# Kernel tuning notes

Hardware: AMD Instinct MI355X
Metric: run time of the kernel (lower is better)

The kernel has to match this reference:

```python
import jax, jax.numpy as jnp
import numpy as np

D_MODEL = 1024
NUM_HEADS = 16
DFF = 4096
LN_EPS = 1e-08
CLIP = 10.0


def setup_inputs() -> dict:
    key = jax.random.key(0)
    ks = jax.random.split(key, 12)
    d, h, f = D_MODEL, NUM_HEADS, DFF
    s = 1.0 / np.sqrt(d)
    inp = {
        "x": jax.random.normal(ks[0], (4, 2048, d), dtype=jnp.float32),
        "wq": jax.random.normal(ks[1], (d, d), dtype=jnp.float32) * s,
        "bq": jnp.zeros((d,), jnp.float32),
        "wk": jax.random.normal(ks[2], (d, d), dtype=jnp.float32) * s,
        "bk": jnp.zeros((d,), jnp.float32),
        "wv": jax.random.normal(ks[3], (d, d), dtype=jnp.float32) * s,
        "bv": jnp.zeros((d,), jnp.float32),
        "wo": jax.random.normal(ks[4], (d, d), dtype=jnp.float32) * s,
        "bo": jnp.zeros((d,), jnp.float32),
        "w1": jax.random.normal(ks[5], (d, f), dtype=jnp.float32) * s,
        "b1": jnp.zeros((f,), jnp.float32),
        "w2": jax.random.normal(ks[6], (f, d), dtype=jnp.float32) * (1.0 / np.sqrt(f)),
        "b2": jnp.zeros((d,), jnp.float32),
        "ln_gamma": jnp.ones((d,), jnp.float32),
        "ln_beta": jnp.zeros((d,), jnp.float32),
    }
    return inp


def layernorm(x, gamma, beta):
    mu = jnp.mean(x, axis=-1, keepdims=True)
    var = jnp.var(x, axis=-1, keepdims=True)
    return (x - mu) * jax.lax.rsqrt(var + LN_EPS) * gamma + beta


def encoder_layer(x, wq, bq, wk, bk, wv, bv, wo, bo, w1, b1, w2, b2, ln_gamma, ln_beta):
    B, S, d = x.shape
    H = NUM_HEADS
    Dh = d // H
    q = (x @ wq + bq).reshape(B, S, H, Dh).transpose(0, 2, 1, 3)  # bhsd
    k = (x @ wk + bk).reshape(B, S, H, Dh).transpose(0, 2, 1, 3)
    v = (x @ wv + bv).reshape(B, S, H, Dh).transpose(0, 2, 1, 3)
    logits = jnp.einsum('bhqd,bhkd->bhqk', q, k) / jnp.sqrt(jnp.float32(Dh))
    logits = jnp.clip(logits, -CLIP, CLIP)
    attn = jax.nn.softmax(logits, axis=-1)
    ctx = jnp.einsum('bhqk,bhkd->bhqd', attn, v)
    ctx = ctx.transpose(0, 2, 1, 3).reshape(B, S, d)
    attn_out = ctx @ wo + bo
    out1 = layernorm(x + attn_out, ln_gamma, ln_beta)
    ffn = jax.nn.relu(out1 @ w1 + b1) @ w2 + b2
    return layernorm(out1 + ffn, ln_gamma, ln_beta)


def reference(x, wq, bq, wk, bk, wv, bv, wo, bo, w1, b1, w2, b2, ln_gamma, ln_beta):
    return encoder_layer(x, wq, bq, wk, bk, wv, bv, wo, bo, w1, b1, w2, b2, ln_gamma, ln_beta)
```

## Files before the change

### kernel.cpp

```cpp
#include <hip/hip_runtime.h>
#include <stdint.h>

#define D_MODEL 1024
#define NHEAD 16
#define DH 64
#define DFF 4096
#define BATCH 4
#define SEQ 2048
#define MTOT (BATCH*SEQ)

#define QSCALE 0.18033688011112043f
#define CLIP2  14.426950408889634f

typedef short short8 __attribute__((ext_vector_type(8)));
typedef float f32x4 __attribute__((ext_vector_type(4)));
typedef unsigned int uint;

__device__ inline unsigned short f2bf(float f) {
  union { float f; unsigned u; } v; v.f = f;
  unsigned r = v.u + 0x7fffu + ((v.u >> 16) & 1u);
  return (unsigned short)(r >> 16);
}
__device__ inline float bf2f(unsigned short b) {
  union { unsigned u; float f; } v; v.u = ((unsigned)b) << 16;
  return v.f;
}
__device__ inline unsigned pack_trunc(float lo, float hi) {
  union { float f; unsigned u; } a, b; a.f = lo; b.f = hi;
  return __builtin_amdgcn_perm(b.u, a.u, 0x07060302u);
}
__device__ __forceinline__ void async16(const unsigned short* g, unsigned short* l) {
  __builtin_amdgcn_global_load_lds(
      (const __attribute__((address_space(1))) unsigned int*)g,
      (__attribute__((address_space(3))) unsigned int*)l, 16, 0, 0);
}

__global__ void cast_kernel(const float* __restrict__ in, unsigned short* __restrict__ out, int n4) {
  int i = blockIdx.x * blockDim.x + threadIdx.x;
  if (i < n4) {
    float4 v = ((const float4*)in)[i];
    ushort4 o;
    o.x = f2bf(v.x); o.y = f2bf(v.y); o.z = f2bf(v.z); o.w = f2bf(v.w);
    ((ushort4*)out)[i] = o;
  }
}

__global__ void transpose_weights_kernel(
    const float* __restrict__ wq, const float* __restrict__ wk,
    const float* __restrict__ wv, const float* __restrict__ wo,
    const float* __restrict__ w1, const float* __restrict__ w2,
    unsigned short* __restrict__ wqkvT, unsigned short* __restrict__ woT,
    unsigned short* __restrict__ w1T, unsigned short* __restrict__ w2T) {
  __shared__ unsigned short tile[32][33];
  const int id = blockIdx.x;
  const float* in; unsigned short* out; int K, N, n0, k0; float scale = 1.0f;
  if (id < 4096) {
    const int wi = id >> 10, t = id & 1023;
    switch (wi) {
      case 0:  in = wq; out = wqkvT;           scale = QSCALE; break;
      case 1:  in = wk; out = wqkvT + 1048576; break;
      case 2:  in = wv; out = wqkvT + 2097152; break;
      default: in = wo; out = woT;             break;
    }
    K = 1024; N = 1024; n0 = (t & 31) * 32; k0 = (t >> 5) * 32;
  } else if (id < 8192) {
    const int t = id - 4096;
    in = w1; out = w1T; K = 1024; N = 4096; n0 = (t & 127) * 32; k0 = (t >> 7) * 32;
  } else {
    const int t = id - 8192;
    in = w2; out = w2T; K = 4096; N = 1024; n0 = (t & 31) * 32; k0 = (t >> 5) * 32;
  }
  const int tx = threadIdx.x & 31, ty = threadIdx.x >> 5;
#pragma unroll
  for (int j = 0; j < 32; j += 8)
    tile[ty + j][tx] = f2bf(in[(size_t)(k0 + ty + j) * N + n0 + tx] * scale);
  __syncthreads();
#pragma unroll
  for (int j = 0; j < 32; j += 8)
    out[(size_t)(n0 + ty + j) * K + k0 + tx] = tile[tx][ty + j];
}

__global__ void bias_concat_kernel(const float* __restrict__ bq, const float* __restrict__ bk,
                                   const float* __restrict__ bv, float* __restrict__ o) {
  int i = blockIdx.x * 256 + threadIdx.x;
  if (i < 3 * D_MODEL) {
    float v = (i < D_MODEL) ? bq[i] * QSCALE
            : (i < 2 * D_MODEL) ? bk[i - D_MODEL] : bv[i - 2 * D_MODEL];
    o[i] = v;
  }
}

__global__ void transpose_v_kernel(const unsigned short* __restrict__ QKV,
                                   unsigned short* __restrict__ Vt) {
  __shared__ unsigned short tile[32][33];
  int bh = blockIdx.z, b = bh >> 4, h = bh & 15;
  int kv0 = blockIdx.x * 32, dh0 = blockIdx.y * 32;
  int tx = threadIdx.x & 31, ty = threadIdx.x >> 5;
#pragma unroll
  for (int j = 0; j < 32; j += 8)
    tile[ty + j][tx] = QKV[(size_t)(b * SEQ + kv0 + ty + j) * 3072 + 2048 + h * DH + dh0 + tx];
  __syncthreads();
#pragma unroll
  for (int j = 0; j < 32; j += 8)
    Vt[(size_t)(bh * DH + dh0 + ty + j) * SEQ + kv0 + tx] = tile[tx][ty + j];
}

template<int RELU, int OUT_BF16, int KSPLIT, int BIAS>
__global__ __launch_bounds__(256, 4) void gemm_bt_kernel(
    const unsigned short* __restrict__ A,
    const unsigned short* __restrict__ Bt,
    const float* __restrict__ bias,
    void* __restrict__ Cout,
    int M, int N, int K) {
  __shared__ __align__(16) unsigned short As[128][32];
  __shared__ __align__(16) unsigned short Bs[128][32];
  const int GX = N >> 7;
  const int xcd = blockIdx.x & 7;
  int li = blockIdx.x >> 3;
  int kh = 0;
  if (KSPLIT == 2) { kh = li & 1; li >>= 1; }
  const int im = xcd * 8 + li / GX;
  const int in_ = li % GX;
  const int m0 = im * 128, n0 = in_ * 128;
  const int tid = threadIdx.x;
  const int wave = tid >> 6, lane = tid & 63;
  const int wm = (wave >> 1) * 64, wn = (wave & 1) * 64;
  const int lm = lane & 15, lq = lane >> 4, lk = (lane >> 4) * 8;
  const int sr = tid >> 2;
  const int sc = (tid & 3) * 8;
  f32x4 acc[4][4] = {};

  const int kbeg = (KSPLIT == 2) ? kh * (K >> 1) : 0;
  const int kend = (KSPLIT == 2) ? kbeg + (K >> 1) : K;
  for (int k0 = kbeg; k0 < kend; k0 += 32) {
    __syncthreads();
#pragma unroll
    for (int s = 0; s < 2; s++) {
      int row = sr + s * 64;
      async16(A  + (size_t)(m0 + row) * K + k0 + sc, &As[0][0] + row * 32 + sc);
      async16(Bt + (size_t)(n0 + row) * K + k0 + sc, &Bs[0][0] + row * 32 + sc);
    }
    __syncthreads();
    short8 af[4], bfr[4];
#pragma unroll
    for (int t = 0; t < 4; t++) {
      af[t]  = *(const short8*)(&As[wm + t * 16 + lm][lk]);
      bfr[t] = *(const short8*)(&Bs[wn + t * 16 + lm][lk]);
    }
#pragma unroll
    for (int mt = 0; mt < 4; mt++)
#pragma unroll
      for (int nt = 0; nt < 4; nt++)
        acc[mt][nt] = __builtin_amdgcn_mfma_f32_16x16x32_bf16(af[mt], bfr[nt], acc[mt][nt], 0, 0, 0);
  }
  unsigned short* Cb = (unsigned short*)Cout + (KSPLIT == 2 ? (size_t)kh * M * N : 0);
#pragma unroll
  for (int nt = 0; nt < 4; nt++) {
    int col = n0 + wn + nt * 16 + lm;
    float bv = BIAS ? bias[col] : 0.0f;
#pragma unroll
    for (int mt = 0; mt < 4; mt++) {
#pragma unroll
      for (int r = 0; r < 4; r++) {
        int row = m0 + wm + mt * 16 + lq * 4 + r;
        float v = acc[mt][nt][r] + bv;
        if (RELU) v = fmaxf(v, 0.0f);
        if (OUT_BF16) Cb[(size_t)row * N + col] = f2bf(v);
        else          ((float*)Cout)[(size_t)row * N + col] = v;
      }
    }
  }
}

__global__ __launch_bounds__(256, 4) void attn_kernel(
    const unsigned short* __restrict__ QKV,
    const unsigned short* __restrict__ Vt_g,
    unsigned short* __restrict__ ctx) {
  __shared__ __align__(16) unsigned short Ks[64 * 64];
  __shared__ __align__(16) unsigned short Vs[64 * 64];
  __shared__ __align__(16) unsigned short Ps[4 * 32 * 64];
  const int bh = blockIdx.x, b = bh >> 4, h = bh & 15;
  const int q0 = blockIdx.y * 128;
  const int tid = threadIdx.x, wave = tid >> 6, lane = tid & 63;
  const int lm = lane & 15, lq = lane >> 4;
  const int srow = tid >> 3, scol = (tid & 7) * 8;
  const int rot = (lm & 7) * 8;

  short8 qf[2][2];
#pragma unroll
  for (int ntq = 0; ntq < 2; ntq++) {
    const unsigned short* qp =
        QKV + (size_t)(b * SEQ + q0 + wave * 32 + ntq * 16 + lm) * 3072 + h * DH;
#pragma unroll
    for (int sl = 0; sl < 2; sl++) qf[ntq][sl] = *(const short8*)(qp + sl * 32 + lq * 8);
  }
  const short8 ones = {0x3F80, 0x3F80, 0x3F80, 0x3F80, 0x3F80, 0x3F80, 0x3F80, 0x3F80};
  f32x4 oacc[2][4] = {};
  f32x4 lsum[2] = {};

  const int sdst = srow * 64 + (scol ^ ((srow & 7) * 8));
  const unsigned short* kg = QKV + (size_t)(b * SEQ) * 3072 + D_MODEL + h * DH + scol;
  const unsigned short* vg = Vt_g + (size_t)(bh * DH + srow) * SEQ + scol;

  uint4 kr0 = *(const uint4*)(kg + (size_t)srow * 3072);
  uint4 kr1 = *(const uint4*)(kg + (size_t)(srow + 32) * 3072);
  uint4 vr0 = *(const uint4*)(vg);
  uint4 vr1 = *(const uint4*)(vg + 32 * SEQ);

  for (int it = 0; it < SEQ / 64; it++) {
    *(uint4*)(Ks + sdst)        = kr0;
    *(uint4*)(Ks + sdst + 2048) = kr1;
    *(uint4*)(Vs + sdst)        = vr0;
    *(uint4*)(Vs + sdst + 2048) = vr1;
    __syncthreads();
    if (it + 1 < SEQ / 64) {
      const int kvn = (it + 1) * 64;
      kr0 = *(const uint4*)(kg + (size_t)(kvn + srow) * 3072);
      kr1 = *(const uint4*)(kg + (size_t)(kvn + srow + 32) * 3072);
      vr0 = *(const uint4*)(vg + kvn);
      vr1 = *(const uint4*)(vg + 32 * SEQ + kvn);
    }

#pragma unroll
    for (int mt = 0; mt < 4; mt++) {
      const unsigned short* krow = Ks + (mt * 16 + lm) * 64;
      short8 kf0 = *(const short8*)(krow + ((lq * 8) ^ rot));
      short8 kf1 = *(const short8*)(krow + ((32 + lq * 8) ^ rot));
#pragma unroll
      for (int ntq = 0; ntq < 2; ntq++) {
        f32x4 sa = {0.f, 0.f, 0.f, 0.f};
        sa = __builtin_amdgcn_mfma_f32_16x16x32_bf16(kf0, qf[ntq][0], sa, 0, 0, 0);
        sa = __builtin_amdgcn_mfma_f32_16x16x32_bf16(kf1, qf[ntq][1], sa, 0, 0, 0);
        float p0 = exp2f(fminf(sa[0], CLIP2));
        float p1 = exp2f(fminf(sa[1], CLIP2));
        float p2 = exp2f(fminf(sa[2], CLIP2));
        float p3 = exp2f(fminf(sa[3], CLIP2));
        uint2 d;
        d.x = pack_trunc(p0, p1);
        d.y = pack_trunc(p2, p3);
        *(uint2*)(Ps + wave * 2048 + (ntq * 16 + lm) * 64 + ((mt * 16 + lq * 4) ^ rot)) = d;
      }
    }
    __builtin_amdgcn_s_waitcnt(0xC07F);
    short8 pf[2][2];
#pragma unroll
    for (int mq = 0; mq < 2; mq++)
#pragma unroll
      for (int sl = 0; sl < 2; sl++)
        pf[mq][sl] = *(const short8*)(Ps + wave * 2048 + (mq * 16 + lm) * 64 + ((sl * 32 + lq * 8) ^ rot));
#pragma unroll
    for (int nt = 0; nt < 4; nt++) {
      const unsigned short* vrow = Vs + (nt * 16 + lm) * 64;
      short8 vf0 = *(const short8*)(vrow + ((lq * 8) ^ rot));
      short8 vf1 = *(const short8*)(vrow + ((32 + lq * 8) ^ rot));
#pragma unroll
      for (int mq = 0; mq < 2; mq++) {
        oacc[mq][nt] = __builtin_amdgcn_mfma_f32_16x16x32_bf16(pf[mq][0], vf0, oacc[mq][nt], 0, 0, 0);
        oacc[mq][nt] = __builtin_amdgcn_mfma_f32_16x16x32_bf16(pf[mq][1], vf1, oacc[mq][nt], 0, 0, 0);
      }
    }
#pragma unroll
    for (int mq = 0; mq < 2; mq++) {
      lsum[mq] = __builtin_amdgcn_mfma_f32_16x16x32_bf16(pf[mq][0], ones, lsum[mq], 0, 0, 0);
      lsum[mq] = __builtin_amdgcn_mfma_f32_16x16x32_bf16(pf[mq][1], ones, lsum[mq], 0, 0, 0);
    }
    __syncthreads();
  }

#pragma unroll
  for (int mq = 0; mq < 2; mq++) {
    float linv[4];
#pragma unroll
    for (int r = 0; r < 4; r++) linv[r] = 1.0f / lsum[mq][r];
    const size_t rowbase =
        (size_t)(b * SEQ + q0 + wave * 32 + mq * 16 + lq * 4) * D_MODEL + h * DH;
#pragma unroll
    for (int nt = 0; nt < 4; nt++) {
#pragma unroll
      for (int r = 0; r < 4; r++) {
        ctx[rowbase + (size_t)r * D_MODEL + nt * 16 + lm] = f2bf(oacc[mq][nt][r] * linv[r]);
      }
    }
  }
}

template<int B_BF16, int WRITE_BF16, int THREE>
__global__ void ln_kernel(const float* __restrict__ A, const void* __restrict__ Bv,
                          const void* __restrict__ B2v, const float* __restrict__ cbias,
                          const float* __restrict__ gamma, const float* __restrict__ beta,
                          float* __restrict__ outf, unsigned short* __restrict__ outb) {
  const int row = blockIdx.x;
  const int tid = threadIdx.x;
  const size_t base = (size_t)row * D_MODEL + tid * 4;
  float4 xa = *(const float4*)(A + base);
  float4 xb;
  if (B_BF16) {
    ushort4 u = *(const ushort4*)((const unsigned short*)Bv + base);
    xb.x = bf2f(u.x); xb.y = bf2f(u.y); xb.z = bf2f(u.z); xb.w = bf2f(u.w);
  } else {
    xb = *(const float4*)((const float*)Bv + base);
  }
  if (THREE) {
    ushort4 u2 = *(const ushort4*)((const unsigned short*)B2v + base);
    float4 cb = *(const float4*)(cbias + tid * 4);
    xb.x += bf2f(u2.x) + cb.x; xb.y += bf2f(u2.y) + cb.y;
    xb.z += bf2f(u2.z) + cb.z; xb.w += bf2f(u2.w) + cb.w;
  }
  float v0 = xa.x + xb.x, v1 = xa.y + xb.y, v2 = xa.z + xb.z, v3 = xa.w + xb.w;
  float s = v0 + v1 + v2 + v3;
  float sq = v0 * v0 + v1 * v1 + v2 * v2 + v3 * v3;
#pragma unroll
  for (int off = 1; off < 64; off <<= 1) {
    s  += __shfl_xor(s, off);
    sq += __shfl_xor(sq, off);
  }
  __shared__ float red[8];
  int wave = tid >> 6;
  if ((tid & 63) == 0) { red[wave * 2] = s; red[wave * 2 + 1] = sq; }
  __syncthreads();
  s  = red[0] + red[2] + red[4] + red[6];
  sq = red[1] + red[3] + red[5] + red[7];
  float mean = s * (1.0f / D_MODEL);
  float var = sq * (1.0f / D_MODEL) - mean * mean;
  float inv = rsqrtf(var + 1e-8f);
  float4 g  = *(const float4*)(gamma + tid * 4);
  float4 be = *(const float4*)(beta + tid * 4);
  float o0 = (v0 - mean) * inv * g.x + be.x;
  float o1 = (v1 - mean) * inv * g.y + be.y;
  float o2 = (v2 - mean) * inv * g.z + be.z;
  float o3 = (v3 - mean) * inv * g.w + be.w;
  float4 of; of.x = o0; of.y = o1; of.z = o2; of.w = o3;
  *(float4*)(outf + base) = of;
  if (WRITE_BF16) {
    ushort4 ub; ub.x = f2bf(o0); ub.y = f2bf(o1); ub.z = f2bf(o2); ub.w = f2bf(o3);
    *(ushort4*)(outb + base) = ub;
  }
}

extern "C" void kernel_launch(void* const* d_in, const int* in_sizes, int n_in,
                              void* d_out, int out_size, void* d_ws, size_t ws_size,
                              hipStream_t stream) {
  const float* x     = (const float*)d_in[0];
  const float* wq    = (const float*)d_in[1];
  const float* bq    = (const float*)d_in[2];
  const float* wk    = (const float*)d_in[3];
  const float* bk    = (const float*)d_in[4];
  const float* wv    = (const float*)d_in[5];
  const float* bv    = (const float*)d_in[6];
  const float* wo    = (const float*)d_in[7];
  const float* bo    = (const float*)d_in[8];
  const float* w1    = (const float*)d_in[9];
  const float* b1    = (const float*)d_in[10];
  const float* w2    = (const float*)d_in[11];
  const float* b2    = (const float*)d_in[12];
  const float* gamma = (const float*)d_in[13];
  const float* beta  = (const float*)d_in[14];

  char* ws = (char*)d_ws;
  const size_t MB = 1ull << 20;
  unsigned short* xb      = (unsigned short*)(ws + 0 * MB);
  unsigned short* out1b   = (unsigned short*)(ws + 0 * MB);
  unsigned short* ffn2    = (unsigned short*)(ws + 0 * MB);
  unsigned short* wqkvT   = (unsigned short*)(ws + 16 * MB);
  unsigned short* woT     = (unsigned short*)(ws + 22 * MB);
  unsigned short* w1T     = (unsigned short*)(ws + 24 * MB);
  unsigned short* w2T     = (unsigned short*)(ws + 32 * MB);
  float*          bqkv    = (float*)(ws + 40 * MB);
  unsigned short* qkvb    = (unsigned short*)(ws + 41 * MB);
  unsigned short* attnoutb= (unsigned short*)(ws + 41 * MB);
  unsigned short* h1      = (unsigned short*)(ws + 41 * MB);
  unsigned short* Vt_g    = (unsigned short*)(ws + 89 * MB);
  unsigned short* ctx     = (unsigned short*)(ws + 105 * MB);
  float*          out1f   = (float*)(ws + 121 * MB);

  cast_kernel<<<(MTOT * D_MODEL / 4 + 255) / 256, 256, 0, stream>>>(x, xb, MTOT * D_MODEL / 4);
  transpose_weights_kernel<<<12288, 256, 0, stream>>>(
      wq, wk, wv, wo, w1, w2, wqkvT, woT, w1T, w2T);
  bias_concat_kernel<<<12, 256, 0, stream>>>(bq, bk, bv, bqkv);

  gemm_bt_kernel<0, 1, 1, 1><<<(3072 / 128) * (MTOT / 128), 256, 0, stream>>>(
      xb, wqkvT, bqkv, qkvb, MTOT, 3072, D_MODEL);
  transpose_v_kernel<<<dim3(SEQ / 32, DH / 32, BATCH * NHEAD), 256, 0, stream>>>(qkvb, Vt_g);
  attn_kernel<<<dim3(BATCH * NHEAD, SEQ / 128), 256, 0, stream>>>(qkvb, Vt_g, ctx);

  gemm_bt_kernel<0, 1, 1, 1><<<(D_MODEL / 128) * (MTOT / 128), 256, 0, stream>>>(
      ctx, woT, bo, attnoutb, MTOT, D_MODEL, D_MODEL);
  ln_kernel<1, 1, 0><<<MTOT, 256, 0, stream>>>(
      x, attnoutb, nullptr, nullptr, gamma, beta, out1f, out1b);
  gemm_bt_kernel<1, 1, 1, 1><<<(DFF / 128) * (MTOT / 128), 256, 0, stream>>>(
      out1b, w1T, b1, h1, MTOT, DFF, D_MODEL);
  gemm_bt_kernel<0, 1, 2, 0><<<2 * (D_MODEL / 128) * (MTOT / 128), 256, 0, stream>>>(
      h1, w2T, nullptr, ffn2, MTOT, D_MODEL, DFF);
  ln_kernel<1, 0, 1><<<MTOT, 256, 0, stream>>>(
      out1f, ffn2, ffn2 + (size_t)MTOT * D_MODEL, b2, gamma, beta, (float*)d_out, nullptr);
}
```

Measured before the change: 574.4 us.

## Add 256x256-tile 8-wave GEMM with ping-pong LDS pipeline for large GEMMs

Introduces a new GEMM kernel using 256x256 output tiles and 512 threads, with double-buffered LDS staging interleaved across four MFMA quadrant phases and barrier- and priority-controlled scheduling. It replaces the 128x128 GEMM for the QKV, FFN1 and FFN2 projections, aiming for higher arithmetic intensity per load and better overlap of global-to-LDS copies with MFMA work. The larger tiles cut the workgroup count and raise register and LDS use (128KB of LDS per block), which can leave fewer tiles to fill the GPU and limit occupancy.

```diff
diff --git a/kernel.cpp b/kernel.cpp
--- a/kernel.cpp
+++ b/kernel.cpp
@@ -172,6 +172,157 @@
   }
 }
 
+#define MFMA_Q(mh, nh)                                                                     \
+  _Pragma("unroll")                                                                        \
+  for (int ks = 0; ks < 2; ks++) {                                                         \
+    _Pragma("unroll")                                                                      \
+    for (int i = 0; i < 4; i++) {                                                          \
+      _Pragma("unroll")                                                                    \
+      for (int nn = 0; nn < 2; nn++) {                                                     \
+        acc[(mh)*4 + i][(nh)*2 + nn] = __builtin_amdgcn_mfma_f32_16x16x32_bf16(            \
+            af[i][ks], bf[(nh)*2 + nn][ks], acc[(mh)*4 + i][(nh)*2 + nn], 0, 0, 0);        \
+      }                                                                                    \
+    }                                                                                      \
+  }
+
+template<int RELU, int OUT_BF16, int KSPLIT, int BIAS>
+__global__ __launch_bounds__(512, 2) void gemm256_bt_kernel(
+    const unsigned short* __restrict__ A,
+    const unsigned short* __restrict__ Bt,
+    const float* __restrict__ bias,
+    void* __restrict__ Cout,
+    int M, int N, int K) {
+  __shared__ __align__(16) unsigned short lds[65536];
+
+  const int nwg = gridDim.x;
+  int nid = (blockIdx.x & 7) * (nwg >> 3) + (blockIdx.x >> 3);
+  int kh = 0;
+  if (KSPLIT == 2) { kh = nid & 1; nid >>= 1; }
+  const int GX = N >> 8;
+  const int im = nid / GX, in_ = nid % GX;
+  const int m0 = im * 256, n0 = in_ * 256;
+
+  const int tid = threadIdx.x;
+  const int lane = tid & 63, wave = tid >> 6;
+  const int wm = (wave >> 2) * 128, wn = (wave & 3) * 64;
+  const int lm = lane & 15, lg = lane >> 4;
+  const int rot = lm & 7;
+  const int aoff0 = ((lg) ^ rot) << 3;
+  const int aoff1 = ((4 + lg) ^ rot) << 3;
+  const int arow = (wm + lm) << 6;
+  const int brow = (wn + lm) << 6;
+
+  const int kbeg = (KSPLIT == 2) ? kh * (K >> 1) : 0;
+  const int nk = ((KSPLIT == 2) ? (K >> 1) : K) >> 6;
+
+  const int rb = tid >> 3;
+  const int gcol = (((tid & 7) ^ (rb & 7)) << 3);
+  const unsigned short* gA = A  + (size_t)(m0 + rb) * K + kbeg + gcol;
+  const unsigned short* gB = Bt + (size_t)(n0 + rb) * K + kbeg + gcol;
+
+  auto stage = [&](const unsigned short* g, int b, int st, unsigned short* seg) {
+    async16(g + (size_t)b * 64 * K + (size_t)st * 64, seg + b * 4096 + tid * 8);
+  };
+
+  f32x4 acc[8][4] = {};
+
+  {
+    unsigned short* A0s = lds;
+    unsigned short* B0s = lds + 16384;
+    unsigned short* A1s = lds + 32768;
+    unsigned short* B1s = lds + 49152;
+    stage(gA, 0, 0, A0s); stage(gA, 2, 0, A0s);
+    stage(gB, 0, 0, B0s); stage(gB, 1, 0, B0s);
+    stage(gA, 1, 0, A0s); stage(gA, 3, 0, A0s);
+    stage(gB, 2, 0, B0s); stage(gB, 3, 0, B0s);
+    stage(gA, 0, 1, A1s); stage(gA, 2, 1, A1s);
+    stage(gB, 0, 1, B1s); stage(gB, 1, 1, B1s);
+    stage(gA, 1, 1, A1s); stage(gA, 3, 1, A1s);
+    __builtin_amdgcn_s_waitcnt(0x0F76);
+    __builtin_amdgcn_s_barrier();
+  }
+
+  for (int t = 0; t < nk; ++t) {
+    const int cur = t & 1;
+    unsigned short* LA = lds + (cur << 15);
+    unsigned short* LB = LA + 16384;
+    unsigned short* NA = lds + ((cur ^ 1) << 15);
+    unsigned short* NB = NA + 16384;
+    short8 af[4][2], bf[4][2];
+
+    if (t + 1 < nk) { stage(gB, 2, t + 1, NB); stage(gB, 3, t + 1, NB); }
+#pragma unroll
+    for (int i = 0; i < 4; i++) {
+      af[i][0] = *(const short8*)(LA + arow + i * 1024 + aoff0);
+      af[i][1] = *(const short8*)(LA + arow + i * 1024 + aoff1);
+    }
+#pragma unroll
+    for (int n = 0; n < 2; n++) {
+      bf[n][0] = *(const short8*)(LB + brow + n * 1024 + aoff0);
+      bf[n][1] = *(const short8*)(LB + brow + n * 1024 + aoff1);
+    }
+    __builtin_amdgcn_s_barrier();
+    __builtin_amdgcn_s_setprio(1);
+    MFMA_Q(0, 0);
+    __builtin_amdgcn_s_setprio(0);
+    __builtin_amdgcn_s_barrier();
+
+    if (t + 2 < nk) { stage(gA, 0, t + 2, LA); stage(gA, 2, t + 2, LA); }
+#pragma unroll
+    for (int n = 2; n < 4; n++) {
+      bf[n][0] = *(const short8*)(LB + brow + n * 1024 + aoff0);
+      bf[n][1] = *(const short8*)(LB + brow + n * 1024 + aoff1);
+    }
+    __builtin_amdgcn_s_barrier();
+    __builtin_amdgcn_s_setprio(1);
+    MFMA_Q(0, 1);
+    __builtin_amdgcn_s_setprio(0);
+    __builtin_amdgcn_s_barrier();
+
+    if (t + 2 < nk) { stage(gB, 0, t + 2, LB); stage(gB, 1, t + 2, LB); }
+#pragma unroll
+    for (int i = 0; i < 4; i++) {
+      af[i][0] = *(const short8*)(LA + arow + 4096 + i * 1024 + aoff0);
+      af[i][1] = *(const short8*)(LA + arow + 4096 + i * 1024 + aoff1);
+    }
+    __builtin_amdgcn_s_barrier();
+    __builtin_amdgcn_s_setprio(1);
+    MFMA_Q(1, 1);
+    __builtin_amdgcn_s_setprio(0);
+    __builtin_amdgcn_s_barrier();
+
+    if (t + 2 < nk) {
+      stage(gA, 1, t + 2, LA); stage(gA, 3, t + 2, LA);
+      __builtin_amdgcn_s_waitcnt(0x0F76);
+    } else {
+      __builtin_amdgcn_s_waitcnt(0x0F70);
+    }
+    __builtin_amdgcn_s_barrier();
+    __builtin_amdgcn_s_setprio(1);
+    MFMA_Q(1, 0);
+    __builtin_amdgcn_s_setprio(0);
+    __builtin_amdgcn_s_barrier();
+  }
+
+  unsigned short* Cb = (unsigned short*)Cout + (KSPLIT == 2 ? (size_t)kh * M * N : 0);
+#pragma unroll
+  for (int nt = 0; nt < 4; nt++) {
+    int col = n0 + wn + nt * 16 + lm;
+    float bv = BIAS ? bias[col] : 0.0f;
+#pragma unroll
+    for (int mf = 0; mf < 8; mf++) {
+#pragma unroll
+      for (int r = 0; r < 4; r++) {
+        int row = m0 + wm + mf * 16 + lg * 4 + r;
+        float v = acc[mf][nt][r] + bv;
+        if (RELU) v = fmaxf(v, 0.0f);
+        if (OUT_BF16) Cb[(size_t)row * N + col] = f2bf(v);
+        else          ((float*)Cout)[(size_t)row * N + col] = v;
+      }
+    }
+  }
+}
+
 __global__ __launch_bounds__(256, 4) void attn_kernel(
     const unsigned short* __restrict__ QKV,
     const unsigned short* __restrict__ Vt_g,
@@ -378,7 +529,7 @@
       wq, wk, wv, wo, w1, w2, wqkvT, woT, w1T, w2T);
   bias_concat_kernel<<<12, 256, 0, stream>>>(bq, bk, bv, bqkv);
 
-  gemm_bt_kernel<0, 1, 1, 1><<<(3072 / 128) * (MTOT / 128), 256, 0, stream>>>(
+  gemm256_bt_kernel<0, 1, 1, 1><<<(3072 / 256) * (MTOT / 256), 512, 0, stream>>>(
       xb, wqkvT, bqkv, qkvb, MTOT, 3072, D_MODEL);
   transpose_v_kernel<<<dim3(SEQ / 32, DH / 32, BATCH * NHEAD), 256, 0, stream>>>(qkvb, Vt_g);
   attn_kernel<<<dim3(BATCH * NHEAD, SEQ / 128), 256, 0, stream>>>(qkvb, Vt_g, ctx);
@@ -387,9 +538,9 @@
       ctx, woT, bo, attnoutb, MTOT, D_MODEL, D_MODEL);
   ln_kernel<1, 1, 0><<<MTOT, 256, 0, stream>>>(
       x, attnoutb, nullptr, nullptr, gamma, beta, out1f, out1b);
-  gemm_bt_kernel<1, 1, 1, 1><<<(DFF / 128) * (MTOT / 128), 256, 0, stream>>>(
+  gemm256_bt_kernel<1, 1, 1, 1><<<(DFF / 256) * (MTOT / 256), 512, 0, stream>>>(
       out1b, w1T, b1, h1, MTOT, DFF, D_MODEL);
-  gemm_bt_kernel<0, 1, 2, 0><<<2 * (D_MODEL / 128) * (MTOT / 128), 256, 0, stream>>>(
+  gemm256_bt_kernel<0, 1, 2, 0><<<2 * (D_MODEL / 256) * (MTOT / 256), 512, 0, stream>>>(
       h1, w2T, nullptr, ffn2, MTOT, D_MODEL, DFF);
   ln_kernel<1, 0, 1><<<MTOT, 256, 0, stream>>>(
       out1f, ffn2, ffn2 + (size_t)MTOT * D_MODEL, b2, gamma, beta, (float*)d_out, nullptr);
```

Result: faster. 543.4 us (-5.4%).
